# Kernel tuning notes

Hardware: AMD Instinct MI355X
Metric: run time of the kernel (lower is better)

Reference implementation:

```python
import jax, jax.numpy as jnp
import numpy as np
from jax import lax

HOPS = 3
B, L, D = 16, 512, 768


def _softmask(x, mask):
    # x: [B,L,L] scores, mask: [B,L] {0,1} floats. Scaled masked softmax per RACL softmask_2d.
    x = x - jnp.max(x, axis=-1, keepdims=True)
    y = jnp.exp(x) * mask[:, None, :]          # mask keys
    att = y / (jnp.sum(y, axis=-1, keepdims=True) + 1e-10)
    return att * mask[:, :, None]              # mask queries


def _conv1d(x, w, b):
    # x: [B,L,D]; w: [D_out, D_in, 3]; conv over L with padding 1 (same length).
    out = lax.conv_general_dilated(jnp.transpose(x, (0, 2, 1)), w, (1,), [(1, 1)],
                                   dimension_numbers=('NCH', 'OIH', 'NCH'))
    return jnp.transpose(out + b[None, :, None], (0, 2, 1))


def _l2norm(x):
    # F.normalize(p=2, dim=-1) with eps=1e-12 (clamp_min)
    return x / jnp.maximum(jnp.linalg.norm(x, axis=-1, keepdims=True), 1e-12)


def setup_inputs() -> dict:
    key = jax.random.key(0)
    ks = jax.random.split(key, 8)
    inputs = jax.random.normal(ks[0], (B, L, D), dtype=jnp.float32)
    mask = jnp.ones((B, L), dtype=jnp.float32)
    conv_w = jax.random.normal(ks[1], (HOPS, D, D, 3), dtype=jnp.float32) * 0.02
    conv_b = jax.random.normal(ks[2], (HOPS, D), dtype=jnp.float32) * 0.02
    pool_w1 = jax.random.normal(ks[3], (D, D), dtype=jnp.float32) * 0.02
    pool_b1 = jax.random.normal(ks[4], (D,), dtype=jnp.float32) * 0.02
    pool_w2 = jax.random.normal(ks[5], (D,), dtype=jnp.float32) * 0.02
    pool_b2 = jax.random.normal(ks[6], (1,), dtype=jnp.float32) * 0.02
    position = jnp.zeros((B, L), dtype=jnp.int64)  # unused by the module
    return {"inputs": inputs, "mask": mask, "conv_w": conv_w, "conv_b": conv_b,
            "pool_w1": pool_w1, "pool_b1": pool_b1, "pool_w2": pool_w2,
            "pool_b2": pool_b2, "position": position}


def reference(inputs, mask, conv_w, conv_b, pool_w1, pool_b1, pool_w2, pool_b2, position):
    att_out = []
    # hop 0: raw (un-normalized) similarity on inputs
    see = jnp.einsum('bld,bmd->blm', inputs, inputs)
    att_out.append(jnp.einsum('blm,bmd->bld', _softmask(see, mask), inputs)[:, :, None, :])
    cur = inputs
    for h in range(HOPS):
        conv = jax.nn.relu(_conv1d(cur, conv_w[h], conv_b[h]))  # dropout = identity (eval)
        n = _l2norm(conv)
        att = _softmask(jnp.einsum('bld,bmd->blm', n, n), mask)  # cosine-sim attention
        att_out.append(jnp.einsum('blm,bmd->bld', att, conv)[:, :, None, :])
        cur = conv
    result = jnp.concatenate(att_out, axis=-2)  # [B,L,HOPS+1,D]
    hidden = jnp.tanh(jnp.einsum('blhd,de->blhe', result, pool_w1) + pool_b1)
    scores = jnp.einsum('blhd,d->blh', hidden, pool_w2) + pool_b2  # [B,L,HOPS+1]
    att_w = jax.nn.softmax(scores, axis=-1)
    weighted = jnp.einsum('blh,blhd->bld', att_w, result)
    return cur, weighted
```

## Files before the change

kernel.cpp:

```cpp
#include <hip/hip_runtime.h>
#include <math.h>

#define B_ 16
#define L_ 512
#define D_ 768
#define HOPS_ 3
#define LK 64

typedef __attribute__((ext_vector_type(8))) short s16x8;
typedef __attribute__((ext_vector_type(4))) short s16x4;
typedef __attribute__((ext_vector_type(4))) float f32x4;

typedef __attribute__((address_space(1))) const unsigned gu32;
typedef __attribute__((address_space(3))) unsigned lu32;

__device__ __forceinline__ void gl16(const void* g, void* l) {
  __builtin_amdgcn_global_load_lds((gu32*)g, (lu32*)l, 16, 0, 0);
}

__device__ __forceinline__ short f2bf(float f) {
  unsigned u = __float_as_uint(f);
  unsigned r = (u + 0x7fffu + ((u >> 16) & 1u)) >> 16;
  return (short)r;
}
__device__ __forceinline__ float bf2f(short s) {
  unsigned u = ((unsigned)(unsigned short)s) << 16;
  return __uint_as_float(u);
}
__device__ __forceinline__ float tanh_fast(float x) {
  float e = __expf(2.f * x);
  return 1.f - 2.f / (e + 1.f);
}

__device__ __forceinline__ s16x8* lds_slot(short (*T)[LK], int row, int slot) {
  return (s16x8*)&T[row][(slot ^ (row & 7)) * 8];
}

__device__ __forceinline__ void mfma4(short (*As)[LK], short (*Bs)[LK],
                                      f32x4 acc[4][4], int wr, int wc, int lq, int lr) {
#pragma unroll
  for (int ks = 0; ks < 2; ++ks) {
    int sl = ks * 4 + lq;
    s16x8 av[4], bv[4];
#pragma unroll
    for (int m = 0; m < 4; ++m) av[m] = *lds_slot(As, wr * 64 + m * 16 + lr, sl);
#pragma unroll
    for (int n = 0; n < 4; ++n) bv[n] = *lds_slot(Bs, wc * 64 + n * 16 + lr, sl);
#pragma unroll
    for (int m = 0; m < 4; ++m)
#pragma unroll
      for (int n = 0; n < 4; ++n)
        acc[m][n] = __builtin_amdgcn_mfma_f32_16x16x32_bf16(av[m], bv[n], acc[m][n], 0, 0, 0);
  }
}

__device__ __forceinline__ void mfma2(short (*As)[LK], short (*Bs)[LK],
                                      f32x4 acc[2][4], int wr, int wc, int lq, int lr) {
#pragma unroll
  for (int ks = 0; ks < 2; ++ks) {
    int sl = ks * 4 + lq;
    s16x8 av[2], bv[4];
#pragma unroll
    for (int m = 0; m < 2; ++m) av[m] = *lds_slot(As, wr * 32 + m * 16 + lr, sl);
#pragma unroll
    for (int n = 0; n < 4; ++n) bv[n] = *lds_slot(Bs, wc * 64 + n * 16 + lr, sl);
#pragma unroll
    for (int m = 0; m < 2; ++m)
#pragma unroll
      for (int n = 0; n < 4; ++n)
        acc[m][n] = __builtin_amdgcn_mfma_f32_16x16x32_bf16(av[m], bv[n], acc[m][n], 0, 0, 0);
  }
}

__device__ __forceinline__ int xcd_remap(int bid, int n) {
  return (bid & 7) * (n >> 3) + (bid >> 3);
}

template <int SPLIT>
__global__ __launch_bounds__(256) void k_sim_mfma(const short* __restrict__ X,
                                                  float* __restrict__ Sout) {
  int wg = xcd_remap(blockIdx.x, gridDim.x);
  int jb = wg & 3, ib = (wg >> 2) & 7, b = wg >> 5;
  int i0 = ib * 64, j0 = jb * 128;
  const int ld = SPLIT ? 1536 : D_;
  const short* Xb = X + (size_t)b * L_ * ld;
  int t = threadIdx.x, lane = t & 63, wid = t >> 6;
  int wr = wid >> 1, wc = wid & 1, lq = lane >> 4, lr = lane & 15;
  __shared__ short As[64][LK];
  __shared__ short Bs[128][LK];
  f32x4 acc[2][4];
#pragma unroll
  for (int m = 0; m < 2; ++m)
#pragma unroll
    for (int n = 0; n < 4; ++n) acc[m][n] = (f32x4){0.f, 0.f, 0.f, 0.f};
  int lrow = lane >> 3;
  int sw = ((lane & 7) ^ lrow) * 8;
  const short* apg[2];
  short* apl[2];
#pragma unroll
  for (int j = 0; j < 2; ++j) {
    apg[j] = Xb + (size_t)(i0 + wid * 16 + j * 8 + lrow) * ld + sw;
    apl[j] = &As[wid * 16 + j * 8][0];
  }
  const short* bpg[4];
  short* bpl[4];
#pragma unroll
  for (int j = 0; j < 4; ++j) {
    bpg[j] = Xb + (size_t)(j0 + wid * 32 + j * 8 + lrow) * ld + sw;
    bpl[j] = &Bs[wid * 32 + j * 8][0];
  }
  const int K = SPLIT ? 2304 : D_;
  for (int k0 = 0; k0 < K; k0 += LK) {
    int seg = SPLIT ? (k0 / 768) : 0;
    int kl = k0 - seg * 768;
    int ak = kl + ((SPLIT && seg == 1) ? 768 : 0);
    int bk = kl + ((SPLIT && seg == 2) ? 768 : 0);
#pragma unroll
    for (int j = 0; j < 2; ++j) gl16(apg[j] + ak, apl[j]);
#pragma unroll
    for (int j = 0; j < 4; ++j) gl16(bpg[j] + bk, bpl[j]);
    __syncthreads();
    mfma2(As, Bs, acc, wr, wc, lq, lr);
    __syncthreads();
  }
  float* Cb = Sout + (size_t)b * L_ * L_;
#pragma unroll
  for (int m = 0; m < 2; ++m)
#pragma unroll
    for (int n = 0; n < 4; ++n)
#pragma unroll
      for (int rr = 0; rr < 4; ++rr)
        Cb[(size_t)(i0 + wr * 32 + m * 16 + 4 * lq + rr) * L_ +
           (j0 + wc * 64 + n * 16 + lr)] = acc[m][n][rr];
}

template <int WF32>
__global__ __launch_bounds__(256) void k_conv_mfma(const short* __restrict__ X, int ldx,
                                                   const short* __restrict__ Wt2,
                                                   const float* __restrict__ bias,
                                                   short* __restrict__ Ybf,
                                                   float* __restrict__ Yf,
                                                   float* __restrict__ rnsq,
                                                   const short* __restrict__ zbuf) {
  int wg = xcd_remap(blockIdx.x, gridDim.x);
  int ob = wg % 6;
  int m_ = wg / 6;
  int b = m_ >> 2, l0 = (m_ & 3) * 128, o0 = ob * 128;
  const short* Xb = X + (size_t)b * L_ * ldx;
  int t = threadIdx.x, lane = t & 63, wid = t >> 6;
  int wr = wid >> 1, wc = wid & 1, lq = lane >> 4, lr = lane & 15;
  __shared__ short As[128][LK];
  __shared__ short Bs[128][LK];
  f32x4 acc[4][4];
#pragma unroll
  for (int m = 0; m < 4; ++m)
#pragma unroll
    for (int n = 0; n < 4; ++n) acc[m][n] = (f32x4){0.f, 0.f, 0.f, 0.f};
  int lrow = lane >> 3;
  int sw = ((lane & 7) ^ lrow) * 8;
  int arow[4];
  const short* bpg[4];
  short* apl[4];
  short* bpl[4];
#pragma unroll
  for (int j = 0; j < 4; ++j) {
    arow[j] = wid * 32 + j * 8 + lrow;
    apl[j] = &As[wid * 32 + j * 8][0];
    bpg[j] = Wt2 + (size_t)(o0 + wid * 32 + j * 8 + lrow) * (3 * D_) + sw;
    bpl[j] = &Bs[wid * 32 + j * 8][0];
  }
  const short* zp = zbuf + sw;
  for (int k0 = 0; k0 < 3 * D_; k0 += LK) {
    int tap = k0 / D_;
    int kl = k0 - tap * D_;
#pragma unroll
    for (int j = 0; j < 4; ++j) {
      int l = l0 + arow[j] + tap - 1;
      const short* src =
          ((unsigned)l < (unsigned)L_) ? Xb + (size_t)l * ldx + kl + sw : zp;
      gl16(src, apl[j]);
    }
#pragma unroll
    for (int j = 0; j < 4; ++j) gl16(bpg[j] + k0, bpl[j]);
    __syncthreads();
    mfma4(As, Bs, acc, wr, wc, lq, lr);
    __syncthreads();
  }
  float bv[4];
#pragma unroll
  for (int n = 0; n < 4; ++n) bv[n] = bias[o0 + wc * 64 + n * 16 + lr];
#pragma unroll
  for (int m = 0; m < 4; ++m)
#pragma unroll
    for (int rr = 0; rr < 4; ++rr) {
      int l = l0 + wr * 64 + m * 16 + 4 * lq + rr;
      size_t rowoff = ((size_t)b * L_ + l) * D_;
      float ss = 0.f;
#pragma unroll
      for (int n = 0; n < 4; ++n) {
        int o = o0 + wc * 64 + n * 16 + lr;
        float v = fmaxf(acc[m][n][rr] + bv[n], 0.f);
        Ybf[rowoff + o] = f2bf(v);
        if (WF32) Yf[rowoff + o] = v;
        ss += v * v;
      }
      ss += __shfl_xor(ss, 1);
      ss += __shfl_xor(ss, 2);
      ss += __shfl_xor(ss, 4);
      ss += __shfl_xor(ss, 8);
      if (lr == 0) atomicAdd(&rnsq[(size_t)b * L_ + l], ss);
    }
}

__global__ __launch_bounds__(256) void k_att_mfma(const short* __restrict__ P,
                                                  const short* __restrict__ Vt,
                                                  short* __restrict__ Rb, int hop) {
  int wg = xcd_remap(blockIdx.x, gridDim.x);
  int db = wg % 6;
  int r2 = wg / 6;
  int b = r2 >> 2, i0 = (r2 & 3) * 128, d0 = db * 128;
  const short* Pb = P + (size_t)b * L_ * L_;
  const short* Vb = Vt + (size_t)b * D_ * L_;
  int t = threadIdx.x, lane = t & 63, wid = t >> 6;
  int wr = wid >> 1, wc = wid & 1, lq = lane >> 4, lr = lane & 15;
  __shared__ short As[128][LK];
  __shared__ short Bs[128][LK];
  f32x4 acc[4][4];
#pragma unroll
  for (int m = 0; m < 4; ++m)
#pragma unroll
    for (int n = 0; n < 4; ++n) acc[m][n] = (f32x4){0.f, 0.f, 0.f, 0.f};
  int lrow = lane >> 3;
  int sw = ((lane & 7) ^ lrow) * 8;
  const short* apg[4];
  const short* bpg[4];
  short* apl[4];
  short* bpl[4];
#pragma unroll
  for (int j = 0; j < 4; ++j) {
    apg[j] = Pb + (size_t)(i0 + wid * 32 + j * 8 + lrow) * L_ + sw;
    apl[j] = &As[wid * 32 + j * 8][0];
    bpg[j] = Vb + (size_t)(d0 + wid * 32 + j * 8 + lrow) * L_ + sw;
    bpl[j] = &Bs[wid * 32 + j * 8][0];
  }
  for (int k0 = 0; k0 < L_; k0 += LK) {
#pragma unroll
    for (int j = 0; j < 4; ++j) gl16(apg[j] + k0, apl[j]);
#pragma unroll
    for (int j = 0; j < 4; ++j) gl16(bpg[j] + k0, bpl[j]);
    __syncthreads();
    mfma4(As, Bs, acc, wr, wc, lq, lr);
    __syncthreads();
  }
#pragma unroll
  for (int m = 0; m < 4; ++m)
#pragma unroll
    for (int n = 0; n < 4; ++n)
#pragma unroll
      for (int rr = 0; rr < 4; ++rr) {
        int i = i0 + wr * 64 + m * 16 + 4 * lq + rr;
        int d = d0 + wc * 64 + n * 16 + lr;
        Rb[((size_t)(b * L_ + i) * 4 + hop) * D_ + d] = f2bf(acc[m][n][rr]);
      }
}

__global__ __launch_bounds__(256) void k_pool_mfma(const short* __restrict__ Rb,
                                                   const short* __restrict__ W1t,
                                                   const float* __restrict__ b1,
                                                   const float* __restrict__ w2,
                                                   float* __restrict__ ps) {
  int wg = xcd_remap(blockIdx.x, gridDim.x);
  int eb = wg % 6;
  int r0 = (wg / 6) * 128, e0 = eb * 128;
  int t = threadIdx.x, lane = t & 63, wid = t >> 6;
  int wr = wid >> 1, wc = wid & 1, lq = lane >> 4, lr = lane & 15;
  __shared__ short As[128][LK];
  __shared__ short Bs[128][LK];
  f32x4 acc[4][4];
#pragma unroll
  for (int m = 0; m < 4; ++m)
#pragma unroll
    for (int n = 0; n < 4; ++n) acc[m][n] = (f32x4){0.f, 0.f, 0.f, 0.f};
  int lrow = lane >> 3;
  int sw = ((lane & 7) ^ lrow) * 8;
  const short* apg[4];
  const short* bpg[4];
  short* apl[4];
  short* bpl[4];
#pragma unroll
  for (int j = 0; j < 4; ++j) {
    apg[j] = Rb + (size_t)(r0 + wid * 32 + j * 8 + lrow) * D_ + sw;
    apl[j] = &As[wid * 32 + j * 8][0];
    bpg[j] = W1t + (size_t)(e0 + wid * 32 + j * 8 + lrow) * D_ + sw;
    bpl[j] = &Bs[wid * 32 + j * 8][0];
  }
  for (int k0 = 0; k0 < D_; k0 += LK) {
#pragma unroll
    for (int j = 0; j < 4; ++j) gl16(apg[j] + k0, apl[j]);
#pragma unroll
    for (int j = 0; j < 4; ++j) gl16(bpg[j] + k0, bpl[j]);
    __syncthreads();
    mfma4(As, Bs, acc, wr, wc, lq, lr);
    __syncthreads();
  }
  float b1v[4], w2v[4];
#pragma unroll
  for (int n = 0; n < 4; ++n) {
    int e = e0 + wc * 64 + n * 16 + lr;
    b1v[n] = b1[e];
    w2v[n] = w2[e];
  }
#pragma unroll
  for (int m = 0; m < 4; ++m)
#pragma unroll
    for (int rr = 0; rr < 4; ++rr) {
      float p = 0.f;
#pragma unroll
      for (int n = 0; n < 4; ++n) p += tanh_fast(acc[m][n][rr] + b1v[n]) * w2v[n];
      p += __shfl_xor(p, 1);
      p += __shfl_xor(p, 2);
      p += __shfl_xor(p, 4);
      p += __shfl_xor(p, 8);
      if (lr == 0) atomicAdd(&ps[r0 + wr * 64 + m * 16 + 4 * lq + rr], p);
    }
}

__global__ __launch_bounds__(256) void k_transp(const short* __restrict__ in, int ld,
                                                short* __restrict__ outT) {
  int l0 = blockIdx.x * 32, d0 = blockIdx.y * 32, b = blockIdx.z;
  __shared__ short tile[32][34];
  int r = threadIdx.x >> 5, c = threadIdx.x & 31;
  const short* ib = in + (size_t)b * L_ * ld;
#pragma unroll
  for (int i = 0; i < 4; ++i)
    tile[r + 8 * i][c] = ib[(size_t)(l0 + r + 8 * i) * ld + d0 + c];
  __syncthreads();
  short* ob = outT + (size_t)b * D_ * L_;
#pragma unroll
  for (int i = 0; i < 4; ++i)
    ob[(size_t)(d0 + r + 8 * i) * L_ + l0 + c] = tile[c][r + 8 * i];
}

template <int NORM>
__global__ __launch_bounds__(256) void k_softmask3(const float* __restrict__ S,
                                                   const float* __restrict__ mask,
                                                   const float* __restrict__ rsq,
                                                   short* __restrict__ P) {
  int b = blockIdx.y;
  int i = blockIdx.x * 4 + (threadIdx.x >> 6);
  int l = threadIdx.x & 63;
  const float* row = S + ((size_t)b * L_ + i) * L_;
  const float* mb = mask + (size_t)b * L_;
  float v[8], mk[8];
  {
    float4 s0 = ((const float4*)row)[l * 2];
    float4 s1 = ((const float4*)row)[l * 2 + 1];
    float4 m0 = ((const float4*)mb)[l * 2];
    float4 m1 = ((const float4*)mb)[l * 2 + 1];
    v[0] = s0.x; v[1] = s0.y; v[2] = s0.z; v[3] = s0.w;
    v[4] = s1.x; v[5] = s1.y; v[6] = s1.z; v[7] = s1.w;
    mk[0] = m0.x; mk[1] = m0.y; mk[2] = m0.z; mk[3] = m0.w;
    mk[4] = m1.x; mk[5] = m1.y; mk[6] = m1.z; mk[7] = m1.w;
  }
  if (NORM) {
    float ri = 1.f / fmaxf(sqrtf(rsq[(size_t)b * L_ + i]), 1e-12f);
    const float4* rq = (const float4*)(rsq + (size_t)b * L_);
    float4 q0 = rq[l * 2], q1 = rq[l * 2 + 1];
    float qq[8] = {q0.x, q0.y, q0.z, q0.w, q1.x, q1.y, q1.z, q1.w};
#pragma unroll
    for (int e = 0; e < 8; ++e) v[e] *= ri / fmaxf(sqrtf(qq[e]), 1e-12f);
  }
  float m = v[0];
#pragma unroll
  for (int e = 1; e < 8; ++e) m = fmaxf(m, v[e]);
#pragma unroll
  for (int s = 1; s < 64; s <<= 1) m = fmaxf(m, __shfl_xor(m, s));
  float y[8], sum = 0.f;
#pragma unroll
  for (int e = 0; e < 8; ++e) {
    y[e] = __expf(v[e] - m) * mk[e];
    sum += y[e];
  }
#pragma unroll
  for (int s = 1; s < 64; s <<= 1) sum += __shfl_xor(sum, s);
  float inv = mb[i] / (sum + 1e-10f);
  s16x8 pk;
#pragma unroll
  for (int e = 0; e < 8; ++e) pk[e] = f2bf(y[e] * inv);
  ((s16x8*)(P + ((size_t)b * L_ + i) * L_))[l] = pk;
}

__global__ void k_prep4(const float* __restrict__ in, short* __restrict__ Xs) {
  size_t idx = (size_t)blockIdx.x * 256 + threadIdx.x;
  if (idx >= (size_t)B_ * L_ * D_ / 4) return;
  float4 x = ((const float4*)in)[idx];
  size_t base = idx * 4;
  size_t bl = base / D_;
  int d = (int)(base % D_);
  float xs[4] = {x.x, x.y, x.z, x.w};
  s16x4 hi, lo;
#pragma unroll
  for (int e = 0; e < 4; ++e) {
    hi[e] = f2bf(xs[e]);
    lo[e] = f2bf(xs[e] - bf2f(hi[e]));
  }
  *(s16x4*)&Xs[bl * 1536 + d] = hi;
  *(s16x4*)&Xs[bl * 1536 + 768 + d] = lo;
}

__global__ void k_wtrans2(const float* __restrict__ w, short* __restrict__ Wt2) {
  size_t idx = (size_t)blockIdx.x * 256 + threadIdx.x;
  const size_t total = (size_t)HOPS_ * D_ * 3 * D_;
  if (idx >= total) return;
  int i = (int)(idx % D_);
  size_t tmp = idx / D_;
  int kk = (int)(tmp % 3);
  tmp /= 3;
  int o = (int)(tmp % D_);
  int h = (int)(tmp / D_);
  Wt2[idx] = f2bf(w[(((size_t)h * D_ + o) * D_ + i) * 3 + kk]);
}

__global__ void k_w1t(const float* __restrict__ W1, short* __restrict__ W1t) {
  size_t idx = (size_t)blockIdx.x * 256 + threadIdx.x;
  if (idx >= (size_t)D_ * D_) return;
  int e = (int)(idx / D_), d = (int)(idx % D_);
  W1t[idx] = f2bf(W1[(size_t)d * D_ + e]);
}

__global__ __launch_bounds__(256) void k_weighted2(const short* __restrict__ Rb,
                                                   const float* __restrict__ ps,
                                                   float* __restrict__ out) {
  int b = blockIdx.y, l = blockIdx.x;
  size_t bl = (size_t)b * L_ + l;
  const float* p = ps + bl * 4;
  float s0 = p[0], s1 = p[1], s2 = p[2], s3 = p[3];
  float m = fmaxf(fmaxf(s0, s1), fmaxf(s2, s3));
  float e0 = __expf(s0 - m), e1 = __expf(s1 - m), e2 = __expf(s2 - m),
        e3 = __expf(s3 - m);
  float inv = 1.f / (e0 + e1 + e2 + e3);
  e0 *= inv; e1 *= inv; e2 *= inv; e3 *= inv;
  const short* Rrow = Rb + bl * 4 * D_;
  float* orow = out + bl * D_;
  for (int d = threadIdx.x; d < D_; d += 256) {
    orow[d] = e0 * bf2f(Rrow[d]) + e1 * bf2f(Rrow[D_ + d]) +
              e2 * bf2f(Rrow[2 * D_ + d]) + e3 * bf2f(Rrow[3 * D_ + d]);
  }
}

extern "C" void kernel_launch(void* const* d_in, const int* in_sizes, int n_in,
                              void* d_out, int out_size, void* d_ws, size_t ws_size,
                              hipStream_t stream) {
  const float* inputs  = (const float*)d_in[0];
  const float* mask    = (const float*)d_in[1];
  const float* conv_w  = (const float*)d_in[2];
  const float* conv_b  = (const float*)d_in[3];
  const float* pool_w1 = (const float*)d_in[4];
  const float* pool_b1 = (const float*)d_in[5];
  const float* pool_w2 = (const float*)d_in[6];
  float* out = (float*)d_out;

  const size_t BLD = (size_t)B_ * L_ * D_;
  const size_t BLL = (size_t)B_ * L_ * L_;

  char* w = (char*)d_ws;
  short* Xs   = (short*)w; w += (size_t)2 * BLD * 2;
  short* Wt2  = (short*)w; w += (size_t)HOPS_ * 3 * D_ * D_ * 2;
  short* W1t  = (short*)w; w += (size_t)D_ * D_ * 2;
  float* S    = (float*)w; w += BLL * 4;
  short* Pb   = (short*)w; w += BLL * 2;
  short* YbfA = (short*)w; w += BLD * 2;
  short* YbfB = (short*)w; w += BLD * 2;
  short* Vt   = (short*)w; w += BLD * 2;
  short* Rb   = (short*)w; w += 4 * BLD * 2;
  float* rnsq = (float*)w; w += (size_t)B_ * L_ * 4;
  float* ps   = (float*)w; w += (size_t)B_ * L_ * 4 * 4;
  short* zbuf = (short*)w; w += 1024;

  hipMemsetAsync(zbuf, 0, 1024, stream);
  k_prep4<<<dim3((unsigned)((BLD / 4 + 255) / 256)), 256, 0, stream>>>(inputs, Xs);
  {
    size_t tot = (size_t)HOPS_ * D_ * 3 * D_;
    k_wtrans2<<<dim3((unsigned)((tot + 255) / 256)), 256, 0, stream>>>(conv_w, Wt2);
  }
  k_w1t<<<dim3((unsigned)(((size_t)D_ * D_ + 255) / 256)), 256, 0, stream>>>(pool_w1, W1t);

  dim3 gtr(L_ / 32, D_ / 32, B_);
  dim3 gsm(L_ / 4, B_);
  dim3 grow(L_, B_);
  const int GSIM = (L_ / 64) * (L_ / 128) * B_;
  const int GCONV = (D_ / 128) * (L_ / 128) * B_;
  const int GATT = GCONV;
  const int GPOOL = (D_ / 128) * (4 * B_ * L_ / 128);

  k_transp<<<gtr, 256, 0, stream>>>(Xs, 1536, Vt);
  k_sim_mfma<1><<<GSIM, 256, 0, stream>>>(Xs, S);
  k_softmask3<0><<<gsm, 256, 0, stream>>>(S, mask, nullptr, Pb);
  k_att_mfma<<<GATT, 256, 0, stream>>>(Pb, Vt, Rb, 0);

  const short* cur = Xs;
  int ldc = 1536;
  for (int h = 0; h < HOPS_; ++h) {
    short* cv = (h & 1) ? YbfB : YbfA;
    const short* Wh = Wt2 + (size_t)h * 3 * D_ * D_;
    const float* bh = conv_b + (size_t)h * D_;
    hipMemsetAsync(rnsq, 0, (size_t)B_ * L_ * sizeof(float), stream);
    if (h == HOPS_ - 1)
      k_conv_mfma<1><<<GCONV, 256, 0, stream>>>(cur, ldc, Wh, bh, cv, out, rnsq, zbuf);
    else
      k_conv_mfma<0><<<GCONV, 256, 0, stream>>>(cur, ldc, Wh, bh, cv, nullptr, rnsq, zbuf);
    k_transp<<<gtr, 256, 0, stream>>>(cv, D_, Vt);
    k_sim_mfma<0><<<GSIM, 256, 0, stream>>>(cv, S);
    k_softmask3<1><<<gsm, 256, 0, stream>>>(S, mask, rnsq, Pb);
    k_att_mfma<<<GATT, 256, 0, stream>>>(Pb, Vt, Rb, h + 1);
    cur = cv;
    ldc = D_;
  }

  hipMemsetAsync(ps, 0, (size_t)B_ * L_ * 4 * sizeof(float), stream);
  k_pool_mfma<<<GPOOL, 256, 0, stream>>>(Rb, W1t, pool_b1, pool_w2, ps);
  k_weighted2<<<grow, 256, 0, stream>>>(Rb, ps, out + BLD);
}
```

Measured before the change: 507.2 us.

## Double-buffer LDS tiles in all MFMA GEMM kernels to overlap loads with compute

Each MFMA GEMM kernel (sim, conv, attention, pool) now keeps two LDS buffers for the A and B tiles. It issues the global-to-LDS loads for the next K-step before running the MFMA work on the current one, and uses one barrier per iteration instead of two. The goal is to hide global load latency behind compute. In exchange, LDS use per block doubles (64 KB for the 128x128 kernels), which may lower occupancy. Correctness relies on the trailing barrier also covering the completion of the async global_load_lds writes.

```diff
diff --git a/kernel.cpp b/kernel.cpp
--- a/kernel.cpp
+++ b/kernel.cpp
@@ -86,8 +86,8 @@
   const short* Xb = X + (size_t)b * L_ * ld;
   int t = threadIdx.x, lane = t & 63, wid = t >> 6;
   int wr = wid >> 1, wc = wid & 1, lq = lane >> 4, lr = lane & 15;
-  __shared__ short As[64][LK];
-  __shared__ short Bs[128][LK];
+  __shared__ short As[2][64][LK];
+  __shared__ short Bs[2][128][LK];
   f32x4 acc[2][4];
 #pragma unroll
   for (int m = 0; m < 2; ++m)
@@ -96,31 +96,31 @@
   int lrow = lane >> 3;
   int sw = ((lane & 7) ^ lrow) * 8;
   const short* apg[2];
-  short* apl[2];
-#pragma unroll
-  for (int j = 0; j < 2; ++j) {
+  const short* bpg[4];
+#pragma unroll
+  for (int j = 0; j < 2; ++j)
     apg[j] = Xb + (size_t)(i0 + wid * 16 + j * 8 + lrow) * ld + sw;
-    apl[j] = &As[wid * 16 + j * 8][0];
-  }
-  const short* bpg[4];
-  short* bpl[4];
-#pragma unroll
-  for (int j = 0; j < 4; ++j) {
+#pragma unroll
+  for (int j = 0; j < 4; ++j)
     bpg[j] = Xb + (size_t)(j0 + wid * 32 + j * 8 + lrow) * ld + sw;
-    bpl[j] = &Bs[wid * 32 + j * 8][0];
-  }
-  const int K = SPLIT ? 2304 : D_;
-  for (int k0 = 0; k0 < K; k0 += LK) {
+
+  auto stage = [&](int p, int k0) {
     int seg = SPLIT ? (k0 / 768) : 0;
     int kl = k0 - seg * 768;
     int ak = kl + ((SPLIT && seg == 1) ? 768 : 0);
     int bk = kl + ((SPLIT && seg == 2) ? 768 : 0);
 #pragma unroll
-    for (int j = 0; j < 2; ++j) gl16(apg[j] + ak, apl[j]);
-#pragma unroll
-    for (int j = 0; j < 4; ++j) gl16(bpg[j] + bk, bpl[j]);
-    __syncthreads();
-    mfma2(As, Bs, acc, wr, wc, lq, lr);
+    for (int j = 0; j < 2; ++j) gl16(apg[j] + ak, &As[p][wid * 16 + j * 8][0]);
+#pragma unroll
+    for (int j = 0; j < 4; ++j) gl16(bpg[j] + bk, &Bs[p][wid * 32 + j * 8][0]);
+  };
+
+  const int NK = (SPLIT ? 2304 : D_) / LK;
+  stage(0, 0);
+  __syncthreads();
+  for (int k = 0; k < NK; ++k) {
+    if (k + 1 < NK) stage((k + 1) & 1, (k + 1) * LK);
+    mfma2(As[k & 1], Bs[k & 1], acc, wr, wc, lq, lr);
     __syncthreads();
   }
   float* Cb = Sout + (size_t)b * L_ * L_;
@@ -149,8 +149,8 @@
   const short* Xb = X + (size_t)b * L_ * ldx;
   int t = threadIdx.x, lane = t & 63, wid = t >> 6;
   int wr = wid >> 1, wc = wid & 1, lq = lane >> 4, lr = lane & 15;
-  __shared__ short As[128][LK];
-  __shared__ short Bs[128][LK];
+  __shared__ short As[2][128][LK];
+  __shared__ short Bs[2][128][LK];
   f32x4 acc[4][4];
 #pragma unroll
   for (int m = 0; m < 4; ++m)
@@ -160,30 +160,33 @@
   int sw = ((lane & 7) ^ lrow) * 8;
   int arow[4];
   const short* bpg[4];
-  short* apl[4];
-  short* bpl[4];
 #pragma unroll
   for (int j = 0; j < 4; ++j) {
-    arow[j] = wid * 32 + j * 8 + lrow;
-    apl[j] = &As[wid * 32 + j * 8][0];
+    arow[j] = l0 + wid * 32 + j * 8 + lrow;
     bpg[j] = Wt2 + (size_t)(o0 + wid * 32 + j * 8 + lrow) * (3 * D_) + sw;
-    bpl[j] = &Bs[wid * 32 + j * 8][0];
   }
   const short* zp = zbuf + sw;
-  for (int k0 = 0; k0 < 3 * D_; k0 += LK) {
+
+  auto stage = [&](int p, int k0) {
     int tap = k0 / D_;
     int kl = k0 - tap * D_;
 #pragma unroll
     for (int j = 0; j < 4; ++j) {
-      int l = l0 + arow[j] + tap - 1;
+      int l = arow[j] + tap - 1;
       const short* src =
           ((unsigned)l < (unsigned)L_) ? Xb + (size_t)l * ldx + kl + sw : zp;
-      gl16(src, apl[j]);
+      gl16(src, &As[p][wid * 32 + j * 8][0]);
     }
 #pragma unroll
-    for (int j = 0; j < 4; ++j) gl16(bpg[j] + k0, bpl[j]);
-    __syncthreads();
-    mfma4(As, Bs, acc, wr, wc, lq, lr);
+    for (int j = 0; j < 4; ++j) gl16(bpg[j] + k0, &Bs[p][wid * 32 + j * 8][0]);
+  };
+
+  const int NK = 3 * D_ / LK;
+  stage(0, 0);
+  __syncthreads();
+  for (int k = 0; k < NK; ++k) {
+    if (k + 1 < NK) stage((k + 1) & 1, (k + 1) * LK);
+    mfma4(As[k & 1], Bs[k & 1], acc, wr, wc, lq, lr);
     __syncthreads();
   }
   float bv[4];
@@ -223,8 +226,8 @@
   const short* Vb = Vt + (size_t)b * D_ * L_;
   int t = threadIdx.x, lane = t & 63, wid = t >> 6;
   int wr = wid >> 1, wc = wid & 1, lq = lane >> 4, lr = lane & 15;
-  __shared__ short As[128][LK];
-  __shared__ short Bs[128][LK];
+  __shared__ short As[2][128][LK];
+  __shared__ short Bs[2][128][LK];
   f32x4 acc[4][4];
 #pragma unroll
   for (int m = 0; m < 4; ++m)
@@ -234,22 +237,24 @@
   int sw = ((lane & 7) ^ lrow) * 8;
   const short* apg[4];
   const short* bpg[4];
-  short* apl[4];
-  short* bpl[4];
 #pragma unroll
   for (int j = 0; j < 4; ++j) {
     apg[j] = Pb + (size_t)(i0 + wid * 32 + j * 8 + lrow) * L_ + sw;
-    apl[j] = &As[wid * 32 + j * 8][0];
     bpg[j] = Vb + (size_t)(d0 + wid * 32 + j * 8 + lrow) * L_ + sw;
-    bpl[j] = &Bs[wid * 32 + j * 8][0];
-  }
-  for (int k0 = 0; k0 < L_; k0 += LK) {
-#pragma unroll
-    for (int j = 0; j < 4; ++j) gl16(apg[j] + k0, apl[j]);
-#pragma unroll
-    for (int j = 0; j < 4; ++j) gl16(bpg[j] + k0, bpl[j]);
-    __syncthreads();
-    mfma4(As, Bs, acc, wr, wc, lq, lr);
+  }
+  auto stage = [&](int p, int k0) {
+#pragma unroll
+    for (int j = 0; j < 4; ++j) gl16(apg[j] + k0, &As[p][wid * 32 + j * 8][0]);
+#pragma unroll
+    for (int j = 0; j < 4; ++j) gl16(bpg[j] + k0, &Bs[p][wid * 32 + j * 8][0]);
+  };
+
+  const int NK = L_ / LK;
+  stage(0, 0);
+  __syncthreads();
+  for (int k = 0; k < NK; ++k) {
+    if (k + 1 < NK) stage((k + 1) & 1, (k + 1) * LK);
+    mfma4(As[k & 1], Bs[k & 1], acc, wr, wc, lq, lr);
     __syncthreads();
   }
 #pragma unroll
@@ -274,8 +279,8 @@
   int r0 = (wg / 6) * 128, e0 = eb * 128;
   int t = threadIdx.x, lane = t & 63, wid = t >> 6;
   int wr = wid >> 1, wc = wid & 1, lq = lane >> 4, lr = lane & 15;
-  __shared__ short As[128][LK];
-  __shared__ short Bs[128][LK];
+  __shared__ short As[2][128][LK];
+  __shared__ short Bs[2][128][LK];
   f32x4 acc[4][4];
 #pragma unroll
   for (int m = 0; m < 4; ++m)
@@ -285,22 +290,24 @@
   int sw = ((lane & 7) ^ lrow) * 8;
   const short* apg[4];
   const short* bpg[4];
-  short* apl[4];
-  short* bpl[4];
 #pragma unroll
   for (int j = 0; j < 4; ++j) {
     apg[j] = Rb + (size_t)(r0 + wid * 32 + j * 8 + lrow) * D_ + sw;
-    apl[j] = &As[wid * 32 + j * 8][0];
     bpg[j] = W1t + (size_t)(e0 + wid * 32 + j * 8 + lrow) * D_ + sw;
-    bpl[j] = &Bs[wid * 32 + j * 8][0];
-  }
-  for (int k0 = 0; k0 < D_; k0 += LK) {
-#pragma unroll
-    for (int j = 0; j < 4; ++j) gl16(apg[j] + k0, apl[j]);
-#pragma unroll
-    for (int j = 0; j < 4; ++j) gl16(bpg[j] + k0, bpl[j]);
-    __syncthreads();
-    mfma4(As, Bs, acc, wr, wc, lq, lr);
+  }
+  auto stage = [&](int p, int k0) {
+#pragma unroll
+    for (int j = 0; j < 4; ++j) gl16(apg[j] + k0, &As[p][wid * 32 + j * 8][0]);
+#pragma unroll
+    for (int j = 0; j < 4; ++j) gl16(bpg[j] + k0, &Bs[p][wid * 32 + j * 8][0]);
+  };
+
+  const int NK = D_ / LK;
+  stage(0, 0);
+  __syncthreads();
+  for (int k = 0; k < NK; ++k) {
+    if (k + 1 < NK) stage((k + 1) & 1, (k + 1) * LK);
+    mfma4(As[k & 1], Bs[k & 1], acc, wr, wc, lq, lr);
     __syncthreads();
   }
   float b1v[4], w2v[4];
```

Result: slower. 527.9 us (+4.1%).

## Fuse V transpose into conv epilogue and merge prep kernels and memsets

Applied to the files above, without the earlier changes.

The conv kernel now writes a bf16 transposed copy of its output (Vt) through a padded shared-memory tile in its epilogue, so the separate transpose kernel after each hop is gone. Input hi/lo split and the first transpose become one prep kernel, and the two weight-conversion kernels become one. Per-hop norm buffers are laid out together so a single memset clears them along with the pool-score buffer and zero buffer, replacing four memsets. This cuts kernel launches and a full re-read of the conv output per hop, at the cost of a longer conv epilogue, an extra barrier and a larger shared-memory footprint.

```diff
diff --git a/kernel.cpp b/kernel.cpp
--- a/kernel.cpp
+++ b/kernel.cpp
@@ -96,19 +96,14 @@
   int lrow = lane >> 3;
   int sw = ((lane & 7) ^ lrow) * 8;
   const short* apg[2];
-  short* apl[2];
-#pragma unroll
-  for (int j = 0; j < 2; ++j) {
+  const short* bpg[4];
+#pragma unroll
+  for (int j = 0; j < 2; ++j)
     apg[j] = Xb + (size_t)(i0 + wid * 16 + j * 8 + lrow) * ld + sw;
-    apl[j] = &As[wid * 16 + j * 8][0];
-  }
-  const short* bpg[4];
-  short* bpl[4];
-#pragma unroll
-  for (int j = 0; j < 4; ++j) {
+#pragma unroll
+  for (int j = 0; j < 4; ++j)
     bpg[j] = Xb + (size_t)(j0 + wid * 32 + j * 8 + lrow) * ld + sw;
-    bpl[j] = &Bs[wid * 32 + j * 8][0];
-  }
+
   const int K = SPLIT ? 2304 : D_;
   for (int k0 = 0; k0 < K; k0 += LK) {
     int seg = SPLIT ? (k0 / 768) : 0;
@@ -116,9 +111,9 @@
     int ak = kl + ((SPLIT && seg == 1) ? 768 : 0);
     int bk = kl + ((SPLIT && seg == 2) ? 768 : 0);
 #pragma unroll
-    for (int j = 0; j < 2; ++j) gl16(apg[j] + ak, apl[j]);
-#pragma unroll
-    for (int j = 0; j < 4; ++j) gl16(bpg[j] + bk, bpl[j]);
+    for (int j = 0; j < 2; ++j) gl16(apg[j] + ak, &As[wid * 16 + j * 8][0]);
+#pragma unroll
+    for (int j = 0; j < 4; ++j) gl16(bpg[j] + bk, &Bs[wid * 32 + j * 8][0]);
     __syncthreads();
     mfma2(As, Bs, acc, wr, wc, lq, lr);
     __syncthreads();
@@ -141,7 +136,8 @@
                                                    short* __restrict__ Ybf,
                                                    float* __restrict__ Yf,
                                                    float* __restrict__ rnsq,
-                                                   const short* __restrict__ zbuf) {
+                                                   const short* __restrict__ zbuf,
+                                                   short* __restrict__ Vt) {
   int wg = xcd_remap(blockIdx.x, gridDim.x);
   int ob = wg % 6;
   int m_ = wg / 6;
@@ -149,8 +145,9 @@
   const short* Xb = X + (size_t)b * L_ * ldx;
   int t = threadIdx.x, lane = t & 63, wid = t >> 6;
   int wr = wid >> 1, wc = wid & 1, lq = lane >> 4, lr = lane & 15;
-  __shared__ short As[128][LK];
-  __shared__ short Bs[128][LK];
+  __shared__ short smem[17408];
+  short (*As)[LK] = (short(*)[LK])smem;
+  short (*Bs)[LK] = (short(*)[LK])(smem + 128 * LK);
   f32x4 acc[4][4];
 #pragma unroll
   for (int m = 0; m < 4; ++m)
@@ -160,28 +157,25 @@
   int sw = ((lane & 7) ^ lrow) * 8;
   int arow[4];
   const short* bpg[4];
-  short* apl[4];
-  short* bpl[4];
 #pragma unroll
   for (int j = 0; j < 4; ++j) {
-    arow[j] = wid * 32 + j * 8 + lrow;
-    apl[j] = &As[wid * 32 + j * 8][0];
+    arow[j] = l0 + wid * 32 + j * 8 + lrow;
     bpg[j] = Wt2 + (size_t)(o0 + wid * 32 + j * 8 + lrow) * (3 * D_) + sw;
-    bpl[j] = &Bs[wid * 32 + j * 8][0];
   }
   const short* zp = zbuf + sw;
+
   for (int k0 = 0; k0 < 3 * D_; k0 += LK) {
     int tap = k0 / D_;
     int kl = k0 - tap * D_;
 #pragma unroll
     for (int j = 0; j < 4; ++j) {
-      int l = l0 + arow[j] + tap - 1;
+      int l = arow[j] + tap - 1;
       const short* src =
           ((unsigned)l < (unsigned)L_) ? Xb + (size_t)l * ldx + kl + sw : zp;
-      gl16(src, apl[j]);
+      gl16(src, &As[wid * 32 + j * 8][0]);
     }
 #pragma unroll
-    for (int j = 0; j < 4; ++j) gl16(bpg[j] + k0, bpl[j]);
+    for (int j = 0; j < 4; ++j) gl16(bpg[j] + k0, &Bs[wid * 32 + j * 8][0]);
     __syncthreads();
     mfma4(As, Bs, acc, wr, wc, lq, lr);
     __syncthreads();
@@ -189,6 +183,13 @@
   float bv[4];
 #pragma unroll
   for (int n = 0; n < 4; ++n) bv[n] = bias[o0 + wc * 64 + n * 16 + lr];
+#pragma unroll
+  for (int m = 0; m < 4; ++m)
+#pragma unroll
+    for (int n = 0; n < 4; ++n)
+#pragma unroll
+      for (int rr = 0; rr < 4; ++rr)
+        acc[m][n][rr] = fmaxf(acc[m][n][rr] + bv[n], 0.f);
 #pragma unroll
   for (int m = 0; m < 4; ++m)
 #pragma unroll
@@ -199,7 +200,7 @@
 #pragma unroll
       for (int n = 0; n < 4; ++n) {
         int o = o0 + wc * 64 + n * 16 + lr;
-        float v = fmaxf(acc[m][n][rr] + bv[n], 0.f);
+        float v = acc[m][n][rr];
         Ybf[rowoff + o] = f2bf(v);
         if (WF32) Yf[rowoff + o] = v;
         ss += v * v;
@@ -210,6 +211,26 @@
       ss += __shfl_xor(ss, 8);
       if (lr == 0) atomicAdd(&rnsq[(size_t)b * L_ + l], ss);
     }
+  short (*T)[136] = (short(*)[136])smem;
+#pragma unroll
+  for (int m = 0; m < 4; ++m)
+#pragma unroll
+    for (int n = 0; n < 4; ++n) {
+      int o_ = wc * 64 + n * 16 + lr;
+      int lb = wr * 64 + m * 16 + 4 * lq;
+      s16x4 pk;
+#pragma unroll
+      for (int rr = 0; rr < 4; ++rr) pk[rr] = f2bf(acc[m][n][rr]);
+      *(s16x4*)&T[o_][lb] = pk;
+    }
+  __syncthreads();
+  short* Vtb = Vt + (size_t)b * D_ * L_;
+#pragma unroll
+  for (int p = 0; p < 8; ++p) {
+    int dl = p * 16 + (t >> 4), lc = (t & 15) * 8;
+    s16x8 q = *(const s16x8*)&T[dl][lc];
+    *(s16x8*)&Vtb[(size_t)(o0 + dl) * L_ + l0 + lc] = q;
+  }
 }
 
 __global__ __launch_bounds__(256) void k_att_mfma(const short* __restrict__ P,
@@ -234,20 +255,16 @@
   int sw = ((lane & 7) ^ lrow) * 8;
   const short* apg[4];
   const short* bpg[4];
-  short* apl[4];
-  short* bpl[4];
 #pragma unroll
   for (int j = 0; j < 4; ++j) {
     apg[j] = Pb + (size_t)(i0 + wid * 32 + j * 8 + lrow) * L_ + sw;
-    apl[j] = &As[wid * 32 + j * 8][0];
     bpg[j] = Vb + (size_t)(d0 + wid * 32 + j * 8 + lrow) * L_ + sw;
-    bpl[j] = &Bs[wid * 32 + j * 8][0];
   }
   for (int k0 = 0; k0 < L_; k0 += LK) {
 #pragma unroll
-    for (int j = 0; j < 4; ++j) gl16(apg[j] + k0, apl[j]);
-#pragma unroll
-    for (int j = 0; j < 4; ++j) gl16(bpg[j] + k0, bpl[j]);
+    for (int j = 0; j < 4; ++j) gl16(apg[j] + k0, &As[wid * 32 + j * 8][0]);
+#pragma unroll
+    for (int j = 0; j < 4; ++j) gl16(bpg[j] + k0, &Bs[wid * 32 + j * 8][0]);
     __syncthreads();
     mfma4(As, Bs, acc, wr, wc, lq, lr);
     __syncthreads();
@@ -285,20 +302,16 @@
   int sw = ((lane & 7) ^ lrow) * 8;
   const short* apg[4];
   const short* bpg[4];
-  short* apl[4];
-  short* bpl[4];
 #pragma unroll
   for (int j = 0; j < 4; ++j) {
     apg[j] = Rb + (size_t)(r0 + wid * 32 + j * 8 + lrow) * D_ + sw;
-    apl[j] = &As[wid * 32 + j * 8][0];
     bpg[j] = W1t + (size_t)(e0 + wid * 32 + j * 8 + lrow) * D_ + sw;
-    bpl[j] = &Bs[wid * 32 + j * 8][0];
   }
   for (int k0 = 0; k0 < D_; k0 += LK) {
 #pragma unroll
-    for (int j = 0; j < 4; ++j) gl16(apg[j] + k0, apl[j]);
-#pragma unroll
-    for (int j = 0; j < 4; ++j) gl16(bpg[j] + k0, bpl[j]);
+    for (int j = 0; j < 4; ++j) gl16(apg[j] + k0, &As[wid * 32 + j * 8][0]);
+#pragma unroll
+    for (int j = 0; j < 4; ++j) gl16(bpg[j] + k0, &Bs[wid * 32 + j * 8][0]);
     __syncthreads();
     mfma4(As, Bs, acc, wr, wc, lq, lr);
     __syncthreads();
@@ -325,20 +338,48 @@
     }
 }
 
-__global__ __launch_bounds__(256) void k_transp(const short* __restrict__ in, int ld,
-                                                short* __restrict__ outT) {
+__global__ __launch_bounds__(256) void k_prep2(const float* __restrict__ in,
+                                               short* __restrict__ Xs,
+                                               short* __restrict__ Vt) {
   int l0 = blockIdx.x * 32, d0 = blockIdx.y * 32, b = blockIdx.z;
-  __shared__ short tile[32][34];
+  __shared__ short tile[32][40];
   int r = threadIdx.x >> 5, c = threadIdx.x & 31;
-  const short* ib = in + (size_t)b * L_ * ld;
-#pragma unroll
-  for (int i = 0; i < 4; ++i)
-    tile[r + 8 * i][c] = ib[(size_t)(l0 + r + 8 * i) * ld + d0 + c];
+  const float* ib = in + ((size_t)b * L_ + l0) * D_ + d0;
+#pragma unroll
+  for (int i = 0; i < 4; ++i) {
+    int rr = r + 8 * i;
+    float x = ib[(size_t)rr * D_ + c];
+    short hi = f2bf(x);
+    short lo = f2bf(x - bf2f(hi));
+    size_t bl = (size_t)b * L_ + l0 + rr;
+    Xs[bl * 1536 + d0 + c] = hi;
+    Xs[bl * 1536 + 768 + d0 + c] = lo;
+    tile[c][rr] = hi;
+  }
   __syncthreads();
-  short* ob = outT + (size_t)b * D_ * L_;
-#pragma unroll
-  for (int i = 0; i < 4; ++i)
-    ob[(size_t)(d0 + r + 8 * i) * L_ + l0 + c] = tile[c][r + 8 * i];
+  int dl = threadIdx.x >> 3, lc = (threadIdx.x & 7) * 4;
+  s16x4 q = *(const s16x4*)&tile[dl][lc];
+  *(s16x4*)&Vt[((size_t)b * D_ + d0 + dl) * L_ + l0 + lc] = q;
+}
+
+__global__ void k_wprep(const float* __restrict__ w, const float* __restrict__ W1,
+                        short* __restrict__ Wt2, short* __restrict__ W1t) {
+  size_t idx = (size_t)blockIdx.x * 256 + threadIdx.x;
+  const size_t tot1 = (size_t)HOPS_ * D_ * 3 * D_;
+  if (idx < tot1) {
+    int i = (int)(idx % D_);
+    size_t tmp = idx / D_;
+    int kk = (int)(tmp % 3);
+    tmp /= 3;
+    int o = (int)(tmp % D_);
+    int h = (int)(tmp / D_);
+    Wt2[idx] = f2bf(w[(((size_t)h * D_ + o) * D_ + i) * 3 + kk]);
+  } else {
+    size_t i2 = idx - tot1;
+    if (i2 >= (size_t)D_ * D_) return;
+    int e = (int)(i2 / D_), d = (int)(i2 % D_);
+    W1t[i2] = f2bf(W1[(size_t)d * D_ + e]);
+  }
 }
 
 template <int NORM>
@@ -390,44 +431,6 @@
   ((s16x8*)(P + ((size_t)b * L_ + i) * L_))[l] = pk;
 }
 
-__global__ void k_prep4(const float* __restrict__ in, short* __restrict__ Xs) {
-  size_t idx = (size_t)blockIdx.x * 256 + threadIdx.x;
-  if (idx >= (size_t)B_ * L_ * D_ / 4) return;
-  float4 x = ((const float4*)in)[idx];
-  size_t base = idx * 4;
-  size_t bl = base / D_;
-  int d = (int)(base % D_);
-  float xs[4] = {x.x, x.y, x.z, x.w};
-  s16x4 hi, lo;
-#pragma unroll
-  for (int e = 0; e < 4; ++e) {
-    hi[e] = f2bf(xs[e]);
-    lo[e] = f2bf(xs[e] - bf2f(hi[e]));
-  }
-  *(s16x4*)&Xs[bl * 1536 + d] = hi;
-  *(s16x4*)&Xs[bl * 1536 + 768 + d] = lo;
-}
-
-__global__ void k_wtrans2(const float* __restrict__ w, short* __restrict__ Wt2) {
-  size_t idx = (size_t)blockIdx.x * 256 + threadIdx.x;
-  const size_t total = (size_t)HOPS_ * D_ * 3 * D_;
-  if (idx >= total) return;
-  int i = (int)(idx % D_);
-  size_t tmp = idx / D_;
-  int kk = (int)(tmp % 3);
-  tmp /= 3;
-  int o = (int)(tmp % D_);
-  int h = (int)(tmp / D_);
-  Wt2[idx] = f2bf(w[(((size_t)h * D_ + o) * D_ + i) * 3 + kk]);
-}
-
-__global__ void k_w1t(const float* __restrict__ W1, short* __restrict__ W1t) {
-  size_t idx = (size_t)blockIdx.x * 256 + threadIdx.x;
-  if (idx >= (size_t)D_ * D_) return;
-  int e = (int)(idx / D_), d = (int)(idx % D_);
-  W1t[idx] = f2bf(W1[(size_t)d * D_ + e]);
-}
-
 __global__ __launch_bounds__(256) void k_weighted2(const short* __restrict__ Rb,
                                                    const float* __restrict__ ps,
                                                    float* __restrict__ out) {
@@ -462,6 +465,7 @@
 
   const size_t BLD = (size_t)B_ * L_ * D_;
   const size_t BLL = (size_t)B_ * L_ * L_;
+  const size_t BL  = (size_t)B_ * L_;
 
   char* w = (char*)d_ws;
   short* Xs   = (short*)w; w += (size_t)2 * BLD * 2;
@@ -473,27 +477,26 @@
   short* YbfB = (short*)w; w += BLD * 2;
   short* Vt   = (short*)w; w += BLD * 2;
   short* Rb   = (short*)w; w += 4 * BLD * 2;
-  float* rnsq = (float*)w; w += (size_t)B_ * L_ * 4;
-  float* ps   = (float*)w; w += (size_t)B_ * L_ * 4 * 4;
+  float* ps   = (float*)w; w += BL * 4 * 4;
+  float* rnsq = (float*)w; w += BL * 3 * 4;
   short* zbuf = (short*)w; w += 1024;
-
-  hipMemsetAsync(zbuf, 0, 1024, stream);
-  k_prep4<<<dim3((unsigned)((BLD / 4 + 255) / 256)), 256, 0, stream>>>(inputs, Xs);
-  {
-    size_t tot = (size_t)HOPS_ * D_ * 3 * D_;
-    k_wtrans2<<<dim3((unsigned)((tot + 255) / 256)), 256, 0, stream>>>(conv_w, Wt2);
-  }
-  k_w1t<<<dim3((unsigned)(((size_t)D_ * D_ + 255) / 256)), 256, 0, stream>>>(pool_w1, W1t);
-
-  dim3 gtr(L_ / 32, D_ / 32, B_);
+  const size_t zero_bytes = BL * 4 * 4 + BL * 3 * 4 + 1024;
+
+  hipMemsetAsync(ps, 0, zero_bytes, stream);
+
+  dim3 gpre(L_ / 32, D_ / 32, B_);
   dim3 gsm(L_ / 4, B_);
   dim3 grow(L_, B_);
   const int GSIM = (L_ / 64) * (L_ / 128) * B_;
   const int GCONV = (D_ / 128) * (L_ / 128) * B_;
   const int GATT = GCONV;
   const int GPOOL = (D_ / 128) * (4 * B_ * L_ / 128);
-
-  k_transp<<<gtr, 256, 0, stream>>>(Xs, 1536, Vt);
+  const size_t wtot = (size_t)HOPS_ * D_ * 3 * D_ + (size_t)D_ * D_;
+
+  k_prep2<<<gpre, 256, 0, stream>>>(inputs, Xs, Vt);
+  k_wprep<<<dim3((unsigned)((wtot + 255) / 256)), 256, 0, stream>>>(conv_w, pool_w1,
+                                                                     Wt2, W1t);
+
   k_sim_mfma<1><<<GSIM, 256, 0, stream>>>(Xs, S);
   k_softmask3<0><<<gsm, 256, 0, stream>>>(S, mask, nullptr, Pb);
   k_att_mfma<<<GATT, 256, 0, stream>>>(Pb, Vt, Rb, 0);
@@ -504,20 +507,18 @@
     short* cv = (h & 1) ? YbfB : YbfA;
     const short* Wh = Wt2 + (size_t)h * 3 * D_ * D_;
     const float* bh = conv_b + (size_t)h * D_;
-    hipMemsetAsync(rnsq, 0, (size_t)B_ * L_ * sizeof(float), stream);
+    float* rq = rnsq + (size_t)h * BL;
     if (h == HOPS_ - 1)
-      k_conv_mfma<1><<<GCONV, 256, 0, stream>>>(cur, ldc, Wh, bh, cv, out, rnsq, zbuf);
+      k_conv_mfma<1><<<GCONV, 256, 0, stream>>>(cur, ldc, Wh, bh, cv, out, rq, zbuf, Vt);
     else
-      k_conv_mfma<0><<<GCONV, 256, 0, stream>>>(cur, ldc, Wh, bh, cv, nullptr, rnsq, zbuf);
-    k_transp<<<gtr, 256, 0, stream>>>(cv, D_, Vt);
+      k_conv_mfma<0><<<GCONV, 256, 0, stream>>>(cur, ldc, Wh, bh, cv, nullptr, rq, zbuf, Vt);
     k_sim_mfma<0><<<GSIM, 256, 0, stream>>>(cv, S);
-    k_softmask3<1><<<gsm, 256, 0, stream>>>(S, mask, rnsq, Pb);
+    k_softmask3<1><<<gsm, 256, 0, stream>>>(S, mask, rq, Pb);
     k_att_mfma<<<GATT, 256, 0, stream>>>(Pb, Vt, Rb, h + 1);
     cur = cv;
     ldc = D_;
   }
 
-  hipMemsetAsync(ps, 0, (size_t)B_ * L_ * 4 * sizeof(float), stream);
   k_pool_mfma<<<GPOOL, 256, 0, stream>>>(Rb, W1t, pool_b1, pool_w2, ps);
   k_weighted2<<<grow, 256, 0, stream>>>(Rb, ps, out + BLD);
 }
```

Result: faster. 483.0 us (-4.8%).
